# Kernel optimization log

Hardware: AMD Instinct MI355X
Metric: run time of the kernel (lower is better)

Reference implementation:

```python
import jax, jax.numpy as jnp
import numpy as np

NUM_NODES = 100000


def setup_inputs() -> dict:
    key = jax.random.key(0)
    k1, k2, k3, k4, k5 = jax.random.split(key, 5)
    E = 3200000
    features = jax.random.normal(k1, (NUM_NODES, 32), dtype=jnp.float32)
    edge_srcs = jax.random.randint(k2, (E,), 0, NUM_NODES, dtype=jnp.int32)
    edge_dsts = jax.random.randint(k3, (E,), 0, NUM_NODES, dtype=jnp.int32)
    edge_weights = jax.random.uniform(k4, (E,), dtype=jnp.float32)
    kernels = jax.random.normal(k5, (32, 32), dtype=jnp.float32) * 0.1
    biases = jnp.zeros((32,), dtype=jnp.float32)
    return {
        "features": features,
        "edge_srcs": edge_srcs,
        "edge_dsts": edge_dsts,
        "edge_weights": edge_weights,
        "kernels": kernels,
        "biases": biases,
    }


def reference(features, edge_srcs, edge_dsts, edge_weights, kernels, biases):
    num_nodes = features.shape[0]
    # dense transform: [N, F_in] @ [F_in, F_out] -> [N, F_out]
    h = features @ kernels
    # per-src degrees via segment sum of ones, clipped to >= 1
    deg = jax.ops.segment_sum(
        jnp.ones_like(edge_srcs, dtype=h.dtype), edge_srcs, num_segments=num_nodes
    )
    norm = jnp.clip(deg, 1.0, None) ** -0.5  # [N]
    # symmetric-normalized edge weights: norm[src] * w * norm[dst]
    w = norm[edge_srcs] * edge_weights * norm[edge_dsts]  # [E]
    # gather dst features, scale, scatter-add into src rows
    nbr = h[edge_dsts] * w[:, None]  # [E, F_out]
    reduced = jax.ops.segment_sum(nbr, edge_srcs, num_segments=num_nodes)
    return reduced + biases
```

## Files before the change

### kernel.cpp

```cpp
#include <hip/hip_runtime.h>
#include <hip/hip_fp16.h>

#define FDIM 32
#define BSH 7
#define BNODES 128
#define NBMAX 1024
#define CHUNK 8192
#define NCMAX 512
#define RCAP 4608
#define SCAP 5120

typedef unsigned int u32;
typedef unsigned short u16;

#define BFLO(u) __uint_as_float((u) << 16)
#define BFHI(u) __uint_as_float((u) & 0xFFFF0000u)

union HCV { __half h; u16 u; };
__device__ __forceinline__ u16 f32_f16b(float f) { HCV c; c.h = __float2half(f); return c.u; }
__device__ __forceinline__ float f16b_f32(u32 b) { HCV c; c.u = (u16)b; return __half2float(c.h); }

__device__ __forceinline__ void acc8(float4& p0, float4& p1, float w, uint4 h) {
    p0.x = fmaf(w, BFLO(h.x), p0.x);
    p0.y = fmaf(w, BFHI(h.x), p0.y);
    p0.z = fmaf(w, BFLO(h.y), p0.z);
    p0.w = fmaf(w, BFHI(h.y), p0.w);
    p1.x = fmaf(w, BFLO(h.z), p1.x);
    p1.y = fmaf(w, BFHI(h.z), p1.y);
    p1.z = fmaf(w, BFLO(h.w), p1.z);
    p1.w = fmaf(w, BFHI(h.w), p1.w);
}

__global__ __launch_bounds__(1024, 8) void k1b(const int* __restrict__ srcs,
                                               const int* __restrict__ dsts,
                                               const float* __restrict__ ew,
                                               u32* __restrict__ offsT,
                                               u32* __restrict__ rkey,
                                               u16* __restrict__ rwh,
                                               int E, int NB, int nch) {
    __shared__ __align__(16) u32 skey[CHUNK];
    __shared__ __align__(16) u16 swv[CHUNK];
    __shared__ u32 lh[NBMAX];
    __shared__ u32 wsum[16];
    int t = threadIdx.x, c = blockIdx.x;
    int base = c * CHUNK;
    int end = base + CHUNK; if (end > E) end = E;
    int nloc = end - base;
    int i0 = t * 8;
    bool full = (i0 + 8 <= nloc);
    int sv[8], dv[8];
    float wv[8];
    u32 rk[8];
    if (full) {
        int4 a  = ((const int4*)(srcs + base))[t * 2];
        int4 b2 = ((const int4*)(srcs + base))[t * 2 + 1];
        int4 d0 = ((const int4*)(dsts + base))[t * 2];
        int4 d1 = ((const int4*)(dsts + base))[t * 2 + 1];
        float4 w0 = ((const float4*)(ew + base))[t * 2];
        float4 w1 = ((const float4*)(ew + base))[t * 2 + 1];
        sv[0]=a.x; sv[1]=a.y; sv[2]=a.z; sv[3]=a.w; sv[4]=b2.x; sv[5]=b2.y; sv[6]=b2.z; sv[7]=b2.w;
        dv[0]=d0.x; dv[1]=d0.y; dv[2]=d0.z; dv[3]=d0.w; dv[4]=d1.x; dv[5]=d1.y; dv[6]=d1.z; dv[7]=d1.w;
        wv[0]=w0.x; wv[1]=w0.y; wv[2]=w0.z; wv[3]=w0.w; wv[4]=w1.x; wv[5]=w1.y; wv[6]=w1.z; wv[7]=w1.w;
    } else {
#pragma unroll
        for (int k = 0; k < 8; ++k) {
            int i = i0 + k;
            bool v = i < nloc;
            sv[k] = v ? srcs[base + i] : 0;
            dv[k] = v ? dsts[base + i] : 0;
            wv[k] = v ? ew[base + i] : 0.f;
        }
    }
    for (int i = t; i < NB; i += 1024) lh[i] = 0u;
    __syncthreads();
    if (full) {
#pragma unroll
        for (int k = 0; k < 8; ++k) rk[k] = atomicAdd(&lh[sv[k] >> BSH], 1u);
    } else {
#pragma unroll
        for (int k = 0; k < 8; ++k) {
            bool v = (i0 + k) < nloc;
            rk[k] = v ? atomicAdd(&lh[sv[k] >> BSH], 1u) : 0u;
        }
    }
    __syncthreads();
    int lane = t & 63, w = t >> 6;
    u32 v = (t < NB) ? lh[t] : 0u;
    u32 inc = v;
#pragma unroll
    for (int d = 1; d < 64; d <<= 1) {
        u32 o = __shfl_up(inc, (unsigned)d, 64);
        if (lane >= d) inc += o;
    }
    if (lane == 63) wsum[w] = inc;
    __syncthreads();
    u32 woff = 0;
    for (int i = 0; i < w; ++i) woff += wsum[i];
    inc += woff;
    u32 ex = inc - v;
    if (t < NB) { offsT[(size_t)t * nch + c] = ex; lh[t] = ex; }
    if (t == 0) offsT[(size_t)NB * nch + c] = (u32)nloc;
    __syncthreads();
    if (full) {
#pragma unroll
        for (int k = 0; k < 8; ++k) {
            int s = sv[k];
            u32 pos = lh[s >> BSH] + rk[k];
            skey[pos] = ((u32)(s & (BNODES - 1)) << 17) | (u32)dv[k];
            swv[pos] = f32_f16b(wv[k]);
        }
    } else {
#pragma unroll
        for (int k = 0; k < 8; ++k) {
            if ((i0 + k) < nloc) {
                int s = sv[k];
                u32 pos = lh[s >> BSH] + rk[k];
                skey[pos] = ((u32)(s & (BNODES - 1)) << 17) | (u32)dv[k];
                swv[pos] = f32_f16b(wv[k]);
            }
        }
    }
    __syncthreads();
    ((uint4*)(rkey + (size_t)base))[t]        = ((const uint4*)skey)[t];
    ((uint4*)(rkey + (size_t)base))[t + 1024] = ((const uint4*)skey)[t + 1024];
    ((uint4*)(rwh + (size_t)base))[t]         = ((const uint4*)swv)[t];
}

__global__ __launch_bounds__(512) void k_sg(const u32* __restrict__ rkey,
                                            const u16* __restrict__ rwh,
                                            const u32* __restrict__ offsT,
                                            const float* __restrict__ feat,
                                            const float* __restrict__ kern,
                                            u32* __restrict__ srec,
                                            u32* __restrict__ nodemeta,
                                            u16* __restrict__ hsb,
                                            int N, int NB, int nch) {
    __shared__ __align__(16) u32 ssrec[SCAP];
    __shared__ float skern[FDIM * FDIM];
    __shared__ float sfeat[BNODES * FDIM];
    __shared__ u32 sbase[NCMAX];
    __shared__ u16 runid[RCAP];
    __shared__ u32 lcnt[BNODES];
    __shared__ u32 lexoff[BNODES];
    __shared__ float lnorm[BNODES];
    __shared__ uint2 ovf[512];
    __shared__ u32 ovn;
    __shared__ u32 wsum[8];
    __shared__ u32 ws2[2];
    __shared__ u32 stot;
    int b = blockIdx.x, t = threadIdx.x;
    int base_n = b << BSH;
    for (int i = t; i < FDIM * FDIM / 4; i += 512) ((float4*)skern)[i] = ((const float4*)kern)[i];
    int base_nf = base_n * FDIM;
    int lim = N * FDIM - base_nf; if (lim > BNODES * FDIM) lim = BNODES * FDIM;
    for (int i = t; i < (lim >> 2); i += 512) ((float4*)sfeat)[i] = ((const float4*)(feat + base_nf))[i];
    if (t < BNODES) lcnt[t] = 0u;
    if (t == 0) ovn = 0u;
    u32 rl = 0u, s0 = 0u;
    if (t < nch) {
        s0 = offsT[(size_t)b * nch + t];
        rl = offsT[(size_t)(b + 1) * nch + t] - s0;
    }
    int lane = t & 63, w = t >> 6;
    u32 inc = rl;
#pragma unroll
    for (int d = 1; d < 64; d <<= 1) {
        u32 o = __shfl_up(inc, (unsigned)d, 64);
        if (lane >= d) inc += o;
    }
    if (lane == 63) wsum[w] = inc;
    __syncthreads();
    u32 woff = 0;
    for (int i = 0; i < w; ++i) woff += wsum[i];
    inc += woff;
    if (t < nch) {
        u32 pl0 = inc - rl;
        sbase[t] = (u32)t * CHUNK + s0 - pl0;
        u32 p = pl0 < RCAP ? pl0 : RCAP;
        u32 e = pl0 + rl; if (e > RCAP) e = RCAP;
        for (; p < e; ++p) runid[p] = (u16)t;
    }
    if (t == nch - 1) stot = inc;
    __syncthreads();
    u32 tot = stot; if (tot > RCAP) tot = RCAP;
    u32 keyv[8], whv[8], rankv[8]; bool val[8];
#pragma unroll
    for (int i = 0; i < 8; ++i) {
        u32 g = (u32)t + ((u32)i << 9);
        val[i] = g < tot;
        keyv[i] = 0u; whv[i] = 0u; rankv[i] = 0u;
        if (val[i]) {
            int r = runid[g];
            u32 idx = sbase[r] + g;
            keyv[i] = rkey[(size_t)idx];
            whv[i] = rwh[(size_t)idx];
        }
    }
#pragma unroll
    for (int i = 0; i < 8; ++i)
        if (val[i]) rankv[i] = atomicAdd(&lcnt[keyv[i] >> 17], 1u);
    for (u32 g = (u32)t + 4096u; g < tot; g += 512u) {
        int r = runid[g];
        u32 idx = sbase[r] + g;
        u32 key = rkey[(size_t)idx];
        u32 wh = rwh[(size_t)idx];
        u32 rk2 = atomicAdd(&lcnt[key >> 17], 1u);
        u32 oi = atomicAdd(&ovn, 1u);
        if (oi < 512u) ovf[oi] = make_uint2(key, (u32)wh | (rk2 << 16));
    }
    __syncthreads();
    u32 d = 0u, pad = 0u, inc2 = 0u;
    if (t < BNODES) {
        d = lcnt[t];
        pad = (d + 3u) & ~3u;
        inc2 = pad;
    }
    if (t < 128) {
#pragma unroll
        for (int dd = 1; dd < 64; dd <<= 1) {
            u32 o = __shfl_up(inc2, (unsigned)dd, 64);
            if ((t & 63) >= dd) inc2 += o;
        }
        if ((t & 63) == 63) ws2[t >> 6] = inc2;
    }
    __syncthreads();
    if (t < 128) {
        if (t >= 64) inc2 += ws2[0];
        u32 ex = inc2 - pad;
        lexoff[t] = ex;
        lnorm[t] = rsqrtf(fmaxf((float)d, 1.0f));
        int n = base_n + t;
        if (n < N) nodemeta[n] = ex | (d << 16);
    }
    __syncthreads();
#pragma unroll
    for (int i = 0; i < 8; ++i) {
        if (val[i]) {
            u32 slot = keyv[i] >> 17;
            u32 pos = lexoff[slot] + rankv[i];
            if (pos < SCAP) ssrec[pos] = ((keyv[i] & 0x1FFFFu) << 15) | ((u32)whv[i] & 0x7FFFu);
        }
    }
    u32 no = ovn; if (no > 512u) no = 512u;
    for (u32 i = t; i < no; i += 512u) {
        uint2 q = ovf[i];
        u32 slot = q.x >> 17;
        u32 pos = lexoff[slot] + (q.y >> 16);
        if (pos < SCAP) ssrec[pos] = ((q.x & 0x1FFFFu) << 15) | (q.y & 0x7FFFu);
    }
    __syncthreads();
    u32* dst = srec + (size_t)b * SCAP;
    for (int i = t; i < SCAP / 4; i += 512) ((uint4*)dst)[i] = ((const uint4*)ssrec)[i];
    int f = t & 31, g8 = t >> 5;
    float kc[FDIM];
#pragma unroll
    for (int k = 0; k < FDIM; ++k) kc[k] = skern[k * FDIM + f];
#pragma unroll
    for (int k8 = 0; k8 < 8; ++k8) {
        int nl = g8 * 8 + k8;
        int n = base_n + nl;
        const float4* fr = (const float4*)(sfeat + nl * FDIM);
        float4 rr[8];
#pragma unroll
        for (int q = 0; q < 8; ++q) rr[q] = fr[q];
        float acc = 0.f;
#pragma unroll
        for (int q = 0; q < 8; ++q) {
            acc = fmaf(rr[q].x, kc[4 * q + 0], acc);
            acc = fmaf(rr[q].y, kc[4 * q + 1], acc);
            acc = fmaf(rr[q].z, kc[4 * q + 2], acc);
            acc = fmaf(rr[q].w, kc[4 * q + 3], acc);
        }
        float x = lnorm[nl] * acc;
        u32 u = __float_as_uint(x);
        u = (u + 0x7FFFu + ((u >> 16) & 1u)) >> 16;
        if (n < N) hsb[(size_t)n * FDIM + f] = (u16)u;
    }
}

__global__ __launch_bounds__(256) void k2(const u32* __restrict__ srec,
                                          const u32* __restrict__ nodemeta,
                                          const u16* __restrict__ hsb,
                                          const float* __restrict__ bias,
                                          float* __restrict__ out,
                                          int N, int NB) {
    __shared__ u32 loff[64];
    __shared__ u32 lcnt[64];
    __shared__ u32 snode[64];
    __shared__ u32 lbin[128];
    __shared__ u32 ws2[2];
    int b2 = blockIdx.x, t = threadIdx.x;
    int b = b2 >> 1, half = b2 & 1;
    int base_n = (b << BSH) + half * 64;
    if (t < 64) {
        int n = base_n + t;
        u32 m = (n < N) ? nodemeta[n] : 0u;
        loff[t] = m & 0xFFFFu;
        lcnt[t] = m >> 16;
    }
    if (t < 128) lbin[t] = 0u;
    __syncthreads();
    if (t < 64) {
        u32 len = lcnt[t];
        atomicAdd(&lbin[len > 127u ? 127u : len], 1u);
    }
    __syncthreads();
    u32 bv_ = 0u, binc = 0u;
    if (t < 128) {
        bv_ = lbin[t];
        binc = bv_;
#pragma unroll
        for (int dd = 1; dd < 64; dd <<= 1) {
            u32 o = __shfl_up(binc, (unsigned)dd, 64);
            if ((t & 63) >= dd) binc += o;
        }
        if ((t & 63) == 63) ws2[t >> 6] = binc;
    }
    __syncthreads();
    if (t < 128) {
        if (t >= 64) binc += ws2[0];
        lbin[t] = binc - bv_;
    }
    __syncthreads();
    if (t < 64) {
        u32 len = lcnt[t];
        u32 pos = atomicAdd(&lbin[len > 127u ? 127u : len], 1u);
        snode[pos] = (u32)t;
    }
    __syncthreads();
    int l = t & 3, g = t >> 2;
    u32 nl = snode[g];
    int n = base_n + (int)nl;
    u32 off = loff[nl];
    u32 len = lcnt[nl];
    float ns = rsqrtf(fmaxf((float)len, 1.0f));
    const u32* sp = srec + (size_t)b * SCAP + off;
    const uint4* hp4 = (const uint4*)hsb;
    float4 bv0 = ((const float4*)bias)[2 * l];
    float4 bv1 = ((const float4*)bias)[2 * l + 1];
    float4 x0 = make_float4(0.f, 0.f, 0.f, 0.f), x1 = make_float4(0.f, 0.f, 0.f, 0.f);
    float4 y0 = make_float4(0.f, 0.f, 0.f, 0.f), y1 = make_float4(0.f, 0.f, 0.f, 0.f);
    u32 j = 0;
    for (; j + 8 <= len; j += 8) {
        uint4 a = *(const uint4*)(sp + j);
        uint4 c = *(const uint4*)(sp + j + 4);
        uint4 h0 = hp4[(size_t)(a.x >> 15) * 4 + l];
        uint4 h1 = hp4[(size_t)(a.y >> 15) * 4 + l];
        uint4 h2 = hp4[(size_t)(a.z >> 15) * 4 + l];
        uint4 h3 = hp4[(size_t)(a.w >> 15) * 4 + l];
        uint4 h4 = hp4[(size_t)(c.x >> 15) * 4 + l];
        uint4 h5 = hp4[(size_t)(c.y >> 15) * 4 + l];
        uint4 h6 = hp4[(size_t)(c.z >> 15) * 4 + l];
        uint4 h7 = hp4[(size_t)(c.w >> 15) * 4 + l];
        acc8(x0, x1, f16b_f32(a.x & 0x7FFFu), h0);
        acc8(y0, y1, f16b_f32(a.y & 0x7FFFu), h1);
        acc8(x0, x1, f16b_f32(a.z & 0x7FFFu), h2);
        acc8(y0, y1, f16b_f32(a.w & 0x7FFFu), h3);
        acc8(x0, x1, f16b_f32(c.x & 0x7FFFu), h4);
        acc8(y0, y1, f16b_f32(c.y & 0x7FFFu), h5);
        acc8(x0, x1, f16b_f32(c.z & 0x7FFFu), h6);
        acc8(y0, y1, f16b_f32(c.w & 0x7FFFu), h7);
    }
    for (; j + 4 <= len; j += 4) {
        uint4 a = *(const uint4*)(sp + j);
        uint4 h0 = hp4[(size_t)(a.x >> 15) * 4 + l];
        uint4 h1 = hp4[(size_t)(a.y >> 15) * 4 + l];
        uint4 h2 = hp4[(size_t)(a.z >> 15) * 4 + l];
        uint4 h3 = hp4[(size_t)(a.w >> 15) * 4 + l];
        acc8(x0, x1, f16b_f32(a.x & 0x7FFFu), h0);
        acc8(y0, y1, f16b_f32(a.y & 0x7FFFu), h1);
        acc8(x0, x1, f16b_f32(a.z & 0x7FFFu), h2);
        acc8(y0, y1, f16b_f32(a.w & 0x7FFFu), h3);
    }
    for (; j < len; ++j) {
        u32 q = sp[j];
        uint4 h = hp4[(size_t)(q >> 15) * 4 + l];
        acc8(x0, x1, f16b_f32(q & 0x7FFFu), h);
    }
    if (n < N) {
        float4 r0, r1;
        r0.x = fmaf(ns, x0.x + y0.x, bv0.x);
        r0.y = fmaf(ns, x0.y + y0.y, bv0.y);
        r0.z = fmaf(ns, x0.z + y0.z, bv0.z);
        r0.w = fmaf(ns, x0.w + y0.w, bv0.w);
        r1.x = fmaf(ns, x1.x + y1.x, bv1.x);
        r1.y = fmaf(ns, x1.y + y1.y, bv1.y);
        r1.z = fmaf(ns, x1.z + y1.z, bv1.z);
        r1.w = fmaf(ns, x1.w + y1.w, bv1.w);
        ((float4*)(out + (size_t)n * FDIM))[2 * l] = r0;
        ((float4*)(out + (size_t)n * FDIM))[2 * l + 1] = r1;
    }
}

extern "C" void kernel_launch(void* const* d_in, const int* in_sizes, int n_in,
                              void* d_out, int out_size, void* d_ws, size_t ws_size,
                              hipStream_t stream) {
    const float* feat = (const float*)d_in[0];
    const int*   srcs = (const int*)d_in[1];
    const int*   dsts = (const int*)d_in[2];
    const float* ew   = (const float*)d_in[3];
    const float* kern = (const float*)d_in[4];
    const float* bias = (const float*)d_in[5];
    float* out = (float*)d_out;

    int N = in_sizes[0] / FDIM;
    int E = in_sizes[1];
    int NB = (N + BNODES - 1) >> BSH;
    int nchunks = (E + CHUNK - 1) / CHUNK;

    char* w = (char*)d_ws;
    u16* hsb      = (u16*)w;   w += (((size_t)N * FDIM * sizeof(u16) + 15) & ~15ull);
    u32* rkey     = (u32*)w;   w += (size_t)nchunks * CHUNK * sizeof(u32);
    u16* rwh      = (u16*)w;   w += (((size_t)nchunks * CHUNK * sizeof(u16) + 15) & ~15ull);
    u32* offsT    = (u32*)w;   w += (size_t)(NB + 1) * nchunks * sizeof(u32);
    u32* nodemeta = (u32*)w;   w += (((size_t)N * sizeof(u32) + 15) & ~15ull);
    u32* srec     = (u32*)w;   w += (size_t)NB * SCAP * sizeof(u32);

    k1b<<<nchunks, 1024, 0, stream>>>(srcs, dsts, ew, offsT, rkey, rwh, E, NB, nchunks);
    k_sg<<<NB, 512, 0, stream>>>(rkey, rwh, offsT, feat, kern, srec, nodemeta, hsb, N, NB, nchunks);
    k2<<<NB * 2, 256, 0, stream>>>(srec, nodemeta, hsb, bias, out, N, NB);
}
```

Before: 170.2 us.

## Split bf16 feature table into column halves and gather in two passes

```diff
diff --git a/kernel.cpp b/kernel.cpp
--- a/kernel.cpp
+++ b/kernel.cpp
@@ -133,7 +133,8 @@
                                             const float* __restrict__ kern,
                                             u32* __restrict__ srec,
                                             u32* __restrict__ nodemeta,
-                                            u16* __restrict__ hsb,
+                                            u16* __restrict__ hsb_lo,
+                                            u16* __restrict__ hsb_hi,
                                             int N, int NB, int nch) {
     __shared__ __align__(16) u32 ssrec[SCAP];
     __shared__ float skern[FDIM * FDIM];
@@ -255,6 +256,8 @@
     float kc[FDIM];
 #pragma unroll
     for (int k = 0; k < FDIM; ++k) kc[k] = skern[k * FDIM + f];
+    u16* hout = (f < 16) ? hsb_lo : hsb_hi;
+    int fo = f & 15;
 #pragma unroll
     for (int k8 = 0; k8 < 8; ++k8) {
         int nl = g8 * 8 + k8;
@@ -274,25 +277,24 @@
         float x = lnorm[nl] * acc;
         u32 u = __float_as_uint(x);
         u = (u + 0x7FFFu + ((u >> 16) & 1u)) >> 16;
-        if (n < N) hsb[(size_t)n * FDIM + f] = (u16)u;
+        if (n < N) hout[(size_t)n * 16 + fo] = (u16)u;
     }
 }
 
-__global__ __launch_bounds__(256) void k2(const u32* __restrict__ srec,
-                                          const u32* __restrict__ nodemeta,
-                                          const u16* __restrict__ hsb,
-                                          const float* __restrict__ bias,
-                                          float* __restrict__ out,
-                                          int N, int NB) {
-    __shared__ u32 loff[64];
-    __shared__ u32 lcnt[64];
-    __shared__ u32 snode[64];
+__global__ __launch_bounds__(256) void k2p(const u32* __restrict__ srec,
+                                           const u32* __restrict__ nodemeta,
+                                           const u16* __restrict__ hsbH,
+                                           const float* __restrict__ bias,
+                                           float* __restrict__ out,
+                                           int N, int colOff) {
+    __shared__ u32 loff[BNODES];
+    __shared__ u32 lcnt[BNODES];
+    __shared__ u32 snode[BNODES];
     __shared__ u32 lbin[128];
     __shared__ u32 ws2[2];
-    int b2 = blockIdx.x, t = threadIdx.x;
-    int b = b2 >> 1, half = b2 & 1;
-    int base_n = (b << BSH) + half * 64;
-    if (t < 64) {
+    int b = blockIdx.x, t = threadIdx.x;
+    int base_n = b << BSH;
+    if (t < BNODES) {
         int n = base_n + t;
         u32 m = (n < N) ? nodemeta[n] : 0u;
         loff[t] = m & 0xFFFFu;
@@ -300,7 +302,7 @@
     }
     if (t < 128) lbin[t] = 0u;
     __syncthreads();
-    if (t < 64) {
+    if (t < BNODES) {
         u32 len = lcnt[t];
         atomicAdd(&lbin[len > 127u ? 127u : len], 1u);
     }
@@ -322,36 +324,36 @@
         lbin[t] = binc - bv_;
     }
     __syncthreads();
-    if (t < 64) {
+    if (t < BNODES) {
         u32 len = lcnt[t];
         u32 pos = atomicAdd(&lbin[len > 127u ? 127u : len], 1u);
         snode[pos] = (u32)t;
     }
     __syncthreads();
-    int l = t & 3, g = t >> 2;
+    int l2 = t & 1, g = t >> 1;
     u32 nl = snode[g];
     int n = base_n + (int)nl;
     u32 off = loff[nl];
     u32 len = lcnt[nl];
     float ns = rsqrtf(fmaxf((float)len, 1.0f));
     const u32* sp = srec + (size_t)b * SCAP + off;
-    const uint4* hp4 = (const uint4*)hsb;
-    float4 bv0 = ((const float4*)bias)[2 * l];
-    float4 bv1 = ((const float4*)bias)[2 * l + 1];
+    const uint4* hp2 = (const uint4*)hsbH;
+    float4 bv0 = *(const float4*)(bias + colOff + 8 * l2);
+    float4 bv1 = *(const float4*)(bias + colOff + 8 * l2 + 4);
     float4 x0 = make_float4(0.f, 0.f, 0.f, 0.f), x1 = make_float4(0.f, 0.f, 0.f, 0.f);
     float4 y0 = make_float4(0.f, 0.f, 0.f, 0.f), y1 = make_float4(0.f, 0.f, 0.f, 0.f);
     u32 j = 0;
     for (; j + 8 <= len; j += 8) {
         uint4 a = *(const uint4*)(sp + j);
         uint4 c = *(const uint4*)(sp + j + 4);
-        uint4 h0 = hp4[(size_t)(a.x >> 15) * 4 + l];
-        uint4 h1 = hp4[(size_t)(a.y >> 15) * 4 + l];
-        uint4 h2 = hp4[(size_t)(a.z >> 15) * 4 + l];
-        uint4 h3 = hp4[(size_t)(a.w >> 15) * 4 + l];
-        uint4 h4 = hp4[(size_t)(c.x >> 15) * 4 + l];
-        uint4 h5 = hp4[(size_t)(c.y >> 15) * 4 + l];
-        uint4 h6 = hp4[(size_t)(c.z >> 15) * 4 + l];
-        uint4 h7 = hp4[(size_t)(c.w >> 15) * 4 + l];
+        uint4 h0 = hp2[(size_t)(a.x >> 15) * 2 + l2];
+        uint4 h1 = hp2[(size_t)(a.y >> 15) * 2 + l2];
+        uint4 h2 = hp2[(size_t)(a.z >> 15) * 2 + l2];
+        uint4 h3 = hp2[(size_t)(a.w >> 15) * 2 + l2];
+        uint4 h4 = hp2[(size_t)(c.x >> 15) * 2 + l2];
+        uint4 h5 = hp2[(size_t)(c.y >> 15) * 2 + l2];
+        uint4 h6 = hp2[(size_t)(c.z >> 15) * 2 + l2];
+        uint4 h7 = hp2[(size_t)(c.w >> 15) * 2 + l2];
         acc8(x0, x1, f16b_f32(a.x & 0x7FFFu), h0);
         acc8(y0, y1, f16b_f32(a.y & 0x7FFFu), h1);
         acc8(x0, x1, f16b_f32(a.z & 0x7FFFu), h2);
@@ -363,10 +365,10 @@
     }
     for (; j + 4 <= len; j += 4) {
         uint4 a = *(const uint4*)(sp + j);
-        uint4 h0 = hp4[(size_t)(a.x >> 15) * 4 + l];
-        uint4 h1 = hp4[(size_t)(a.y >> 15) * 4 + l];
-        uint4 h2 = hp4[(size_t)(a.z >> 15) * 4 + l];
-        uint4 h3 = hp4[(size_t)(a.w >> 15) * 4 + l];
+        uint4 h0 = hp2[(size_t)(a.x >> 15) * 2 + l2];
+        uint4 h1 = hp2[(size_t)(a.y >> 15) * 2 + l2];
+        uint4 h2 = hp2[(size_t)(a.z >> 15) * 2 + l2];
+        uint4 h3 = hp2[(size_t)(a.w >> 15) * 2 + l2];
         acc8(x0, x1, f16b_f32(a.x & 0x7FFFu), h0);
         acc8(y0, y1, f16b_f32(a.y & 0x7FFFu), h1);
         acc8(x0, x1, f16b_f32(a.z & 0x7FFFu), h2);
@@ -374,7 +376,7 @@
     }
     for (; j < len; ++j) {
         u32 q = sp[j];
-        uint4 h = hp4[(size_t)(q >> 15) * 4 + l];
+        uint4 h = hp2[(size_t)(q >> 15) * 2 + l2];
         acc8(x0, x1, f16b_f32(q & 0x7FFFu), h);
     }
     if (n < N) {
@@ -387,8 +389,9 @@
         r1.y = fmaf(ns, x1.y + y1.y, bv1.y);
         r1.z = fmaf(ns, x1.z + y1.z, bv1.z);
         r1.w = fmaf(ns, x1.w + y1.w, bv1.w);
-        ((float4*)(out + (size_t)n * FDIM))[2 * l] = r0;
-        ((float4*)(out + (size_t)n * FDIM))[2 * l + 1] = r1;
+        float* op = out + (size_t)n * FDIM + colOff + 8 * l2;
+        *(float4*)op = r0;
+        *(float4*)(op + 4) = r1;
     }
 }
 
@@ -409,7 +412,8 @@
     int nchunks = (E + CHUNK - 1) / CHUNK;
 
     char* w = (char*)d_ws;
-    u16* hsb      = (u16*)w;   w += (((size_t)N * FDIM * sizeof(u16) + 15) & ~15ull);
+    u16* hsb_lo   = (u16*)w;   w += (((size_t)N * 16 * sizeof(u16) + 15) & ~15ull);
+    u16* hsb_hi   = (u16*)w;   w += (((size_t)N * 16 * sizeof(u16) + 15) & ~15ull);
     u32* rkey     = (u32*)w;   w += (size_t)nchunks * CHUNK * sizeof(u32);
     u16* rwh      = (u16*)w;   w += (((size_t)nchunks * CHUNK * sizeof(u16) + 15) & ~15ull);
     u32* offsT    = (u32*)w;   w += (size_t)(NB + 1) * nchunks * sizeof(u32);
@@ -417,6 +421,7 @@
     u32* srec     = (u32*)w;   w += (size_t)NB * SCAP * sizeof(u32);
 
     k1b<<<nchunks, 1024, 0, stream>>>(srcs, dsts, ew, offsT, rkey, rwh, E, NB, nchunks);
-    k_sg<<<NB, 512, 0, stream>>>(rkey, rwh, offsT, feat, kern, srec, nodemeta, hsb, N, NB, nchunks);
-    k2<<<NB * 2, 256, 0, stream>>>(srec, nodemeta, hsb, bias, out, N, NB);
+    k_sg<<<NB, 512, 0, stream>>>(rkey, rwh, offsT, feat, kern, srec, nodemeta, hsb_lo, hsb_hi, N, NB, nchunks);
+    k2p<<<NB, 256, 0, stream>>>(srec, nodemeta, hsb_lo, bias, out, N, 0);
+    k2p<<<NB, 256, 0, stream>>>(srec, nodemeta, hsb_hi, bias, out, N, 16);
 }
```

Result: slower. 193.2 us (+13.5%).
